# Performance work log

Hardware: AMD Instinct MI355X
Metric: run time of the kernel (lower is better)

Reference implementation:

```python
import jax, jax.numpy as jnp
import numpy as np

N, E, F_IN, HEADS, OUT_PER_HEAD = 50000, 1600000, 128, 4, 32
NEG_SLOPE = 0.2  # LeakyReLU slope used by standard GATConv


def setup_inputs() -> dict:
    key = jax.random.key(0)
    ks = jax.random.split(key, 7)
    x = jax.random.normal(ks[0], (N, F_IN), dtype=jnp.float32)
    edge_src = jax.random.randint(ks[1], (E,), 0, N, dtype=jnp.int64)
    edge_dst = jax.random.randint(ks[2], (E,), 0, N, dtype=jnp.int64)
    W = jax.random.normal(ks[3], (F_IN, HEADS * OUT_PER_HEAD), dtype=jnp.float32) / np.float32(np.sqrt(F_IN))
    a_src = jax.random.normal(ks[4], (HEADS, OUT_PER_HEAD), dtype=jnp.float32) * 0.1
    a_dst = jax.random.normal(ks[5], (HEADS, OUT_PER_HEAD), dtype=jnp.float32) * 0.1
    bias = jnp.zeros((HEADS * OUT_PER_HEAD,), dtype=jnp.float32)
    return {"x": x, "W": W, "a_src": a_src, "a_dst": a_dst, "bias": bias,
            "edge_src": edge_src, "edge_dst": edge_dst}


def reference(x, W, a_src, a_dst, bias, edge_src, edge_dst):
    # GATConv with concat=True over a static edge list (the faithful
    # static-shape form of tf.where(adj>0.5) -> gather -> GAT -> scatter).
    n = x.shape[0]
    H, D = a_src.shape
    h = (x @ W).reshape(n, H, D)                      # [N,H,D] projected features
    # per-node attention logits for source / destination roles
    e_s = jnp.einsum('nhd,hd->nh', h, a_src)          # [N,H]
    e_d = jnp.einsum('nhd,hd->nh', h, a_dst)          # [N,H]
    # per-edge logits with LeakyReLU
    e = jax.nn.leaky_relu(e_s[edge_src] + e_d[edge_dst], NEG_SLOPE)  # [E,H]
    # numerically stable softmax over incoming edges of each destination node
    m = jax.ops.segment_max(e, edge_dst, num_segments=n)             # [N,H]
    m = jnp.where(jnp.isfinite(m), m, 0.0)
    alpha = jnp.exp(e - m[edge_dst])                                 # [E,H]
    denom = jax.ops.segment_sum(alpha, edge_dst, num_segments=n)     # [N,H]
    alpha = alpha / jnp.where(denom > 0, denom, 1.0)[edge_dst]
    # weighted aggregation of source features onto destinations
    msgs = alpha[:, :, None] * h[edge_src]                           # [E,H,D]
    out = jax.ops.segment_sum(msgs, edge_dst, num_segments=n)        # [N,H,D]
    return out.reshape(n, H * D) + bias
```

## Files before the change

### kernel.cpp

```cpp
#include <hip/hip_runtime.h>
#include <math.h>

#define NEG_SLOPE 0.2f
#define NB1 256
#define XROW 136
#define BSHIFT 4
#define BNODES 16
#define CAP 1024
#define NBUCK_MAX 3200

typedef __attribute__((ext_vector_type(8))) short short8;
typedef __attribute__((ext_vector_type(4))) float floatx4;

__device__ __forceinline__ unsigned short f2bf(float f) {
    unsigned int u = __float_as_uint(f);
    u += 0x7fffu + ((u >> 16) & 1u);
    return (unsigned short)(u >> 16);
}
__device__ __forceinline__ float bf2f(unsigned short b) {
    return __uint_as_float(((unsigned int)b) << 16);
}
__device__ __forceinline__ float u2fl(unsigned int u) {
    return __uint_as_float(u << 16);
}
__device__ __forceinline__ float u2fh(unsigned int u) {
    return __uint_as_float(u & 0xffff0000u);
}

__device__ __forceinline__ void fma8(float* a, int o, float wt, const uint4& hv) {
    a[o + 0] = fmaf(wt, u2fl(hv.x), a[o + 0]);
    a[o + 1] = fmaf(wt, u2fh(hv.x), a[o + 1]);
    a[o + 2] = fmaf(wt, u2fl(hv.y), a[o + 2]);
    a[o + 3] = fmaf(wt, u2fh(hv.y), a[o + 3]);
    a[o + 4] = fmaf(wt, u2fl(hv.z), a[o + 4]);
    a[o + 5] = fmaf(wt, u2fh(hv.z), a[o + 5]);
    a[o + 6] = fmaf(wt, u2fl(hv.w), a[o + 6]);
    a[o + 7] = fmaf(wt, u2fh(hv.w), a[o + 7]);
}

__global__ __launch_bounds__(256) void prep_w_kernel(
    const float* __restrict__ W, unsigned short* __restrict__ WThi,
    unsigned short* __restrict__ WTlo, int* __restrict__ gcur, int nbuck)
{
    const int idx = blockIdx.x * 256 + threadIdx.x;
    const int j = idx >> 7, k = idx & 127;
    const float w = W[k * 128 + j];
    const unsigned short hi = f2bf(w);
    const unsigned short lo = f2bf(w - bf2f(hi));
    WThi[idx] = hi;
    WTlo[idx] = lo;
    if (idx < nbuck) gcur[idx] = idx * CAP;
}

__global__ __launch_bounds__(256) void fused_gemm_scatter(
    const float* __restrict__ x, const unsigned short* __restrict__ WThi,
    const unsigned short* __restrict__ WTlo, const float* __restrict__ a_src,
    const float* __restrict__ a_dst, unsigned short* __restrict__ hb,
    float* __restrict__ es, float* __restrict__ ed, int n,
    const int* __restrict__ src, const int* __restrict__ dst,
    int* __restrict__ gcur, int* __restrict__ ebuf, int e, int nbuck)
{
    __shared__ union {
        struct { unsigned short Xhi[32 * XROW]; unsigned short Xlo[32 * XROW]; } g;
        int cnt[NBUCK_MAX];
    } sm;

    const int t = threadIdx.x;

    if (blockIdx.x < NB1) {
        for (int b = t; b < nbuck; b += 256) sm.cnt[b] = 0;
        __syncthreads();
        const int per = (e + NB1 - 1) / NB1;
        const int lo = blockIdx.x * per;
        const int m = min(e, lo + per) - lo;
        for (int j = t; j < m; j += 256)
            atomicAdd(&sm.cnt[dst[lo + j] >> BSHIFT], 1);
        __syncthreads();
        for (int b = t; b < nbuck; b += 256) {
            const int c = sm.cnt[b];
            if (c > 0) sm.cnt[b] = atomicAdd(&gcur[b], c);
        }
        __syncthreads();
        for (int j = t; j < m; j += 256) {
            const int d = dst[lo + j];
            const int pos = atomicAdd(&sm.cnt[d >> BSHIFT], 1);
            ebuf[pos] = src[lo + j] | ((d & (BNODES - 1)) << 16);
        }
        return;
    }

    const int wv = t >> 6, lane = t & 63;
    const int l16 = lane & 15, quad = lane >> 4;
    const int node_base = (blockIdx.x - NB1) * 32;

    short8 bh[4][2], bl[4][2];
    #pragma unroll
    for (int c = 0; c < 4; ++c) {
        #pragma unroll
        for (int u = 0; u < 2; ++u) {
            const int j = (wv * 2 + u) * 16 + l16;
            const int ko = c * 32 + quad * 8;
            bh[c][u] = *(const short8*)&WThi[j * 128 + ko];
            bl[c][u] = *(const short8*)&WTlo[j * 128 + ko];
        }
    }

    for (int i = t; i < 1024; i += 256) {
        const int nd = i >> 5;
        const int k4 = i & 31;
        float4 xv = make_float4(0.f, 0.f, 0.f, 0.f);
        if (node_base + nd < n)
            xv = ((const float4*)(x + (size_t)(node_base + nd) * 128))[k4];
        const unsigned short h0 = f2bf(xv.x), h1 = f2bf(xv.y),
                             h2 = f2bf(xv.z), h3 = f2bf(xv.w);
        const unsigned short l0 = f2bf(xv.x - bf2f(h0)), l1 = f2bf(xv.y - bf2f(h1)),
                             l2 = f2bf(xv.z - bf2f(h2)), l3 = f2bf(xv.w - bf2f(h3));
        *(ushort4*)&sm.g.Xhi[nd * XROW + k4 * 4] = make_ushort4(h0, h1, h2, h3);
        *(ushort4*)&sm.g.Xlo[nd * XROW + k4 * 4] = make_ushort4(l0, l1, l2, l3);
    }
    __syncthreads();

    floatx4 acc[2][2] = {};
    #pragma unroll
    for (int c = 0; c < 4; ++c) {
        const int ko = c * 32 + quad * 8;
        short8 ah[2], al[2];
        #pragma unroll
        for (int r = 0; r < 2; ++r) {
            ah[r] = *(const short8*)&sm.g.Xhi[(r * 16 + l16) * XROW + ko];
            al[r] = *(const short8*)&sm.g.Xlo[(r * 16 + l16) * XROW + ko];
        }
        #pragma unroll
        for (int r = 0; r < 2; ++r)
        #pragma unroll
        for (int u = 0; u < 2; ++u) {
            acc[r][u] = __builtin_amdgcn_mfma_f32_16x16x32_bf16(ah[r], bl[c][u], acc[r][u], 0, 0, 0);
            acc[r][u] = __builtin_amdgcn_mfma_f32_16x16x32_bf16(al[r], bh[c][u], acc[r][u], 0, 0, 0);
            acc[r][u] = __builtin_amdgcn_mfma_f32_16x16x32_bf16(ah[r], bh[c][u], acc[r][u], 0, 0, 0);
        }
    }

    float asv[2], adv[2];
    #pragma unroll
    for (int u = 0; u < 2; ++u) {
        const int feat = (wv * 2 + u) * 16 + l16;
        asv[u] = a_src[feat];
        adv[u] = a_dst[feat];
    }
    #pragma unroll
    for (int r = 0; r < 2; ++r) {
        #pragma unroll
        for (int u = 0; u < 2; ++u) {
            const int feat = (wv * 2 + u) * 16 + l16;
            #pragma unroll
            for (int g = 0; g < 4; ++g) {
                const int node = node_base + r * 16 + quad * 4 + g;
                if (node < n)
                    hb[(size_t)node * 128 + feat] = f2bf(acc[r][u][g]);
            }
        }
        #pragma unroll
        for (int g = 0; g < 4; ++g) {
            float ps = acc[r][0][g] * asv[0] + acc[r][1][g] * asv[1];
            float pd = acc[r][0][g] * adv[0] + acc[r][1][g] * adv[1];
            #pragma unroll
            for (int o = 8; o >= 1; o >>= 1) {
                ps += __shfl_xor(ps, o);
                pd += __shfl_xor(pd, o);
            }
            const int node = node_base + r * 16 + quad * 4 + g;
            if (l16 == 0 && node < n) {
                es[node * 4 + wv] = ps;
                ed[node * 4 + wv] = pd;
            }
        }
    }
}

__global__ __launch_bounds__(256) void sort_agg_kernel(
    const unsigned short* __restrict__ hb, const float* __restrict__ es,
    const float* __restrict__ ed, const float* __restrict__ bias,
    const int* __restrict__ gcur, const int* __restrict__ ebuf,
    float* __restrict__ out, int n)
{
    __shared__ unsigned short esort[CAP];
    __shared__ int hist[BNODES], hexcl[BNODES], cur[BNODES];
    const int b = blockIdx.x;
    const int t = threadIdx.x;
    const int lane = t & 63;
    const int wv = t >> 6;
    const int l8 = lane & 7;
    const int oct = lane >> 3;
    const int f0 = l8 * 16;
    const int hh = l8 >> 1;

    const int start = b * CAP;
    const int end = gcur[b];

    if (t < BNODES) hist[t] = 0;
    __syncthreads();
    for (int i = start + t; i < end; i += 256)
        atomicAdd(&hist[(ebuf[i] >> 16) & (BNODES - 1)], 1);
    __syncthreads();
    if (wv == 0) {
        const int v = (lane < BNODES) ? hist[lane] : 0;
        int incl = v;
        #pragma unroll
        for (int o = 1; o < BNODES; o <<= 1) {
            const int tt = __shfl_up(incl, o);
            if (lane >= o) incl += tt;
        }
        if (lane < BNODES) { hexcl[lane] = incl - v; cur[lane] = incl - v; }
    }
    __syncthreads();
    for (int i = start + t; i < end; i += 256) {
        const int v = ebuf[i];
        const int pos = atomicAdd(&cur[(v >> 16) & (BNODES - 1)], 1);
        esort[pos] = (unsigned short)(v & 0xFFFF);
    }
    __syncthreads();

    for (int j = 0; j < 4; ++j) {
        const int nd = wv * 4 + j;
        const int node = b * BNODES + nd;
        if (node >= n) break;
        const int off = hexcl[nd];
        const int deg = hist[nd];
        const float edh = ed[(size_t)node * 4 + hh];

        float a[16];
        #pragma unroll
        for (int k = 0; k < 16; ++k) a[k] = 0.f;
        float wsum = 0.f;

        for (int c0 = 0; c0 < deg; c0 += 16) {
            const int ci0 = c0 + oct;
            const int ci1 = ci0 + 8;
            const int dm = deg - 1;
            const int s0 = esort[off + min(ci0, dm)];
            const int s1 = esort[off + min(ci1, dm)];
            const float e0 = es[(size_t)s0 * 4 + hh];
            const float e1 = es[(size_t)s1 * 4 + hh];
            const uint4 hA0 = *(const uint4*)&hb[(size_t)s0 * 128 + f0];
            const uint4 hB0 = *(const uint4*)&hb[(size_t)s0 * 128 + f0 + 8];
            const uint4 hA1 = *(const uint4*)&hb[(size_t)s1 * 128 + f0];
            const uint4 hB1 = *(const uint4*)&hb[(size_t)s1 * 128 + f0 + 8];
            float lg0 = e0 + edh; lg0 = lg0 > 0.f ? lg0 : NEG_SLOPE * lg0;
            float lg1 = e1 + edh; lg1 = lg1 > 0.f ? lg1 : NEG_SLOPE * lg1;
            const float w0 = (ci0 < deg) ? __expf(lg0) : 0.f;
            const float w1 = (ci1 < deg) ? __expf(lg1) : 0.f;
            fma8(a, 0, w0, hA0); fma8(a, 8, w0, hB0);
            fma8(a, 0, w1, hA1); fma8(a, 8, w1, hB1);
            wsum += w0 + w1;
        }
        #pragma unroll
        for (int o = 8; o <= 32; o <<= 1) {
            #pragma unroll
            for (int k = 0; k < 16; ++k) a[k] += __shfl_xor(a[k], o);
            wsum += __shfl_xor(wsum, o);
        }
        if (oct == 0) {
            const float inv = 1.f / ((wsum > 0.f) ? wsum : 1.f);
            #pragma unroll
            for (int q = 0; q < 4; ++q) {
                const float4 bq = *(const float4*)(bias + f0 + q * 4);
                float4 o4;
                o4.x = a[q * 4 + 0] * inv + bq.x;
                o4.y = a[q * 4 + 1] * inv + bq.y;
                o4.z = a[q * 4 + 2] * inv + bq.z;
                o4.w = a[q * 4 + 3] * inv + bq.w;
                *(float4*)(out + (size_t)node * 128 + f0 + q * 4) = o4;
            }
        }
    }
}

extern "C" void kernel_launch(void* const* d_in, const int* in_sizes, int n_in,
                              void* d_out, int out_size, void* d_ws, size_t ws_size,
                              hipStream_t stream)
{
    const float* x      = (const float*)d_in[0];
    const float* W      = (const float*)d_in[1];
    const float* a_src  = (const float*)d_in[2];
    const float* a_dst  = (const float*)d_in[3];
    const float* bias   = (const float*)d_in[4];
    const int*   e_src  = (const int*)d_in[5];
    const int*   e_dst  = (const int*)d_in[6];
    float* out = (float*)d_out;

    const int n = in_sizes[0] / 128;
    const int e = in_sizes[5];
    const int nbuck = (n + BNODES - 1) >> BSHIFT;

    char* ws = (char*)d_ws;
    size_t o = 0;
    auto alloc = [&](size_t bytes) { void* p = ws + o; o += (bytes + 255) & ~(size_t)255; return p; };
    unsigned short* hb   = (unsigned short*)alloc((size_t)n * 128 * sizeof(unsigned short));
    unsigned short* WThi = (unsigned short*)alloc(128 * 128 * sizeof(unsigned short));
    unsigned short* WTlo = (unsigned short*)alloc(128 * 128 * sizeof(unsigned short));
    float* es      = (float*)alloc((size_t)n * 4 * sizeof(float));
    float* ed      = (float*)alloc((size_t)n * 4 * sizeof(float));
    int* gcur      = (int*)alloc((size_t)nbuck * sizeof(int));
    int* ebuf      = (int*)alloc((size_t)nbuck * CAP * sizeof(int));
    (void)ws_size; (void)n_in; (void)out_size;

    const int ngemm = (n + 31) / 32;
    prep_w_kernel<<<64, 256, 0, stream>>>(W, WThi, WTlo, gcur, nbuck);
    fused_gemm_scatter<<<NB1 + ngemm, 256, 0, stream>>>(x, WThi, WTlo, a_src, a_dst,
                                                        hb, es, ed, n,
                                                        e_src, e_dst, gcur, ebuf, e, nbuck);
    sort_agg_kernel<<<nbuck, 256, 0, stream>>>(hb, es, ed, bias, gcur, ebuf, out, n);
}
```

Before: 195.7 us.

## Replace shared-memory bucket histogram scatter with per-edge global atomics spread over all blocks

Edge bucketing no longer runs in 256 dedicated blocks that build a shared-memory histogram, reserve ranges with one global atomic per bucket, then scatter. Every block now does its GEMM tile and then bucket-scatters 1024 edges, using one global atomicAdd per edge on the bucket cursor. This spreads the scatter over far more blocks, drops the large shared histogram so occupancy can rise, and removes the three-phase barrier structure. In exchange it issues 1.6M contended global atomics instead of block-aggregated ones, and it makes the order of edges within each bucket nondeterministic.

```diff
diff --git a/kernel.cpp b/kernel.cpp
--- a/kernel.cpp
+++ b/kernel.cpp
@@ -2,12 +2,11 @@
 #include <math.h>
 
 #define NEG_SLOPE 0.2f
-#define NB1 256
 #define XROW 136
 #define BSHIFT 4
 #define BNODES 16
 #define CAP 1024
-#define NBUCK_MAX 3200
+#define EPB 1024
 
 typedef __attribute__((ext_vector_type(8))) short short8;
 typedef __attribute__((ext_vector_type(4))) float floatx4;
@@ -58,120 +57,120 @@
     const float* __restrict__ a_dst, unsigned short* __restrict__ hb,
     float* __restrict__ es, float* __restrict__ ed, int n,
     const int* __restrict__ src, const int* __restrict__ dst,
-    int* __restrict__ gcur, int* __restrict__ ebuf, int e, int nbuck)
+    int* __restrict__ gcur, int* __restrict__ ebuf, int e)
 {
-    __shared__ union {
-        struct { unsigned short Xhi[32 * XROW]; unsigned short Xlo[32 * XROW]; } g;
-        int cnt[NBUCK_MAX];
-    } sm;
-
+    __shared__ unsigned short Xhi[32 * XROW];
+    __shared__ unsigned short Xlo[32 * XROW];
     const int t = threadIdx.x;
-
-    if (blockIdx.x < NB1) {
-        for (int b = t; b < nbuck; b += 256) sm.cnt[b] = 0;
-        __syncthreads();
-        const int per = (e + NB1 - 1) / NB1;
-        const int lo = blockIdx.x * per;
-        const int m = min(e, lo + per) - lo;
-        for (int j = t; j < m; j += 256)
-            atomicAdd(&sm.cnt[dst[lo + j] >> BSHIFT], 1);
-        __syncthreads();
-        for (int b = t; b < nbuck; b += 256) {
-            const int c = sm.cnt[b];
-            if (c > 0) sm.cnt[b] = atomicAdd(&gcur[b], c);
-        }
-        __syncthreads();
-        for (int j = t; j < m; j += 256) {
-            const int d = dst[lo + j];
-            const int pos = atomicAdd(&sm.cnt[d >> BSHIFT], 1);
-            ebuf[pos] = src[lo + j] | ((d & (BNODES - 1)) << 16);
-        }
-        return;
-    }
-
     const int wv = t >> 6, lane = t & 63;
     const int l16 = lane & 15, quad = lane >> 4;
-    const int node_base = (blockIdx.x - NB1) * 32;
-
-    short8 bh[4][2], bl[4][2];
-    #pragma unroll
-    for (int c = 0; c < 4; ++c) {
-        #pragma unroll
-        for (int u = 0; u < 2; ++u) {
-            const int j = (wv * 2 + u) * 16 + l16;
+    const int node_base = blockIdx.x * 32;
+
+    if (node_base < n) {
+        short8 bh[4][2], bl[4][2];
+        #pragma unroll
+        for (int c = 0; c < 4; ++c) {
+            #pragma unroll
+            for (int u = 0; u < 2; ++u) {
+                const int j = (wv * 2 + u) * 16 + l16;
+                const int ko = c * 32 + quad * 8;
+                bh[c][u] = *(const short8*)&WThi[j * 128 + ko];
+                bl[c][u] = *(const short8*)&WTlo[j * 128 + ko];
+            }
+        }
+
+        for (int i = t; i < 1024; i += 256) {
+            const int nd = i >> 5;
+            const int k4 = i & 31;
+            float4 xv = make_float4(0.f, 0.f, 0.f, 0.f);
+            if (node_base + nd < n)
+                xv = ((const float4*)(x + (size_t)(node_base + nd) * 128))[k4];
+            const unsigned short h0 = f2bf(xv.x), h1 = f2bf(xv.y),
+                                 h2 = f2bf(xv.z), h3 = f2bf(xv.w);
+            const unsigned short l0 = f2bf(xv.x - bf2f(h0)), l1 = f2bf(xv.y - bf2f(h1)),
+                                 l2 = f2bf(xv.z - bf2f(h2)), l3 = f2bf(xv.w - bf2f(h3));
+            *(ushort4*)&Xhi[nd * XROW + k4 * 4] = make_ushort4(h0, h1, h2, h3);
+            *(ushort4*)&Xlo[nd * XROW + k4 * 4] = make_ushort4(l0, l1, l2, l3);
+        }
+        __syncthreads();
+
+        floatx4 acc[2][2] = {};
+        #pragma unroll
+        for (int c = 0; c < 4; ++c) {
             const int ko = c * 32 + quad * 8;
-            bh[c][u] = *(const short8*)&WThi[j * 128 + ko];
-            bl[c][u] = *(const short8*)&WTlo[j * 128 + ko];
-        }
-    }
-
-    for (int i = t; i < 1024; i += 256) {
-        const int nd = i >> 5;
-        const int k4 = i & 31;
-        float4 xv = make_float4(0.f, 0.f, 0.f, 0.f);
-        if (node_base + nd < n)
-            xv = ((const float4*)(x + (size_t)(node_base + nd) * 128))[k4];
-        const unsigned short h0 = f2bf(xv.x), h1 = f2bf(xv.y),
-                             h2 = f2bf(xv.z), h3 = f2bf(xv.w);
-        const unsigned short l0 = f2bf(xv.x - bf2f(h0)), l1 = f2bf(xv.y - bf2f(h1)),
-                             l2 = f2bf(xv.z - bf2f(h2)), l3 = f2bf(xv.w - bf2f(h3));
-        *(ushort4*)&sm.g.Xhi[nd * XROW + k4 * 4] = make_ushort4(h0, h1, h2, h3);
-        *(ushort4*)&sm.g.Xlo[nd * XROW + k4 * 4] = make_ushort4(l0, l1, l2, l3);
-    }
-    __syncthreads();
-
-    floatx4 acc[2][2] = {};
-    #pragma unroll
-    for (int c = 0; c < 4; ++c) {
-        const int ko = c * 32 + quad * 8;
-        short8 ah[2], al[2];
-        #pragma unroll
-        for (int r = 0; r < 2; ++r) {
-            ah[r] = *(const short8*)&sm.g.Xhi[(r * 16 + l16) * XROW + ko];
-            al[r] = *(const short8*)&sm.g.Xlo[(r * 16 + l16) * XROW + ko];
-        }
-        #pragma unroll
-        for (int r = 0; r < 2; ++r)
-        #pragma unroll
-        for (int u = 0; u < 2; ++u) {
-            acc[r][u] = __builtin_amdgcn_mfma_f32_16x16x32_bf16(ah[r], bl[c][u], acc[r][u], 0, 0, 0);
-            acc[r][u] = __builtin_amdgcn_mfma_f32_16x16x32_bf16(al[r], bh[c][u], acc[r][u], 0, 0, 0);
-            acc[r][u] = __builtin_amdgcn_mfma_f32_16x16x32_bf16(ah[r], bh[c][u], acc[r][u], 0, 0, 0);
-        }
-    }
-
-    float asv[2], adv[2];
-    #pragma unroll
-    for (int u = 0; u < 2; ++u) {
-        const int feat = (wv * 2 + u) * 16 + l16;
-        asv[u] = a_src[feat];
-        adv[u] = a_dst[feat];
-    }
-    #pragma unroll
-    for (int r = 0; r < 2; ++r) {
+            short8 ah[2], al[2];
+            #pragma unroll
+            for (int r = 0; r < 2; ++r) {
+                ah[r] = *(const short8*)&Xhi[(r * 16 + l16) * XROW + ko];
+                al[r] = *(const short8*)&Xlo[(r * 16 + l16) * XROW + ko];
+            }
+            #pragma unroll
+            for (int r = 0; r < 2; ++r)
+            #pragma unroll
+            for (int u = 0; u < 2; ++u) {
+                acc[r][u] = __builtin_amdgcn_mfma_f32_16x16x32_bf16(ah[r], bl[c][u], acc[r][u], 0, 0, 0);
+                acc[r][u] = __builtin_amdgcn_mfma_f32_16x16x32_bf16(al[r], bh[c][u], acc[r][u], 0, 0, 0);
+                acc[r][u] = __builtin_amdgcn_mfma_f32_16x16x32_bf16(ah[r], bh[c][u], acc[r][u], 0, 0, 0);
+            }
+        }
+
+        float asv[2], adv[2];
         #pragma unroll
         for (int u = 0; u < 2; ++u) {
             const int feat = (wv * 2 + u) * 16 + l16;
+            asv[u] = a_src[feat];
+            adv[u] = a_dst[feat];
+        }
+        #pragma unroll
+        for (int r = 0; r < 2; ++r) {
+            #pragma unroll
+            for (int u = 0; u < 2; ++u) {
+                const int feat = (wv * 2 + u) * 16 + l16;
+                #pragma unroll
+                for (int g = 0; g < 4; ++g) {
+                    const int node = node_base + r * 16 + quad * 4 + g;
+                    if (node < n)
+                        hb[(size_t)node * 128 + feat] = f2bf(acc[r][u][g]);
+                }
+            }
             #pragma unroll
             for (int g = 0; g < 4; ++g) {
+                float ps = acc[r][0][g] * asv[0] + acc[r][1][g] * asv[1];
+                float pd = acc[r][0][g] * adv[0] + acc[r][1][g] * adv[1];
+                #pragma unroll
+                for (int o = 8; o >= 1; o >>= 1) {
+                    ps += __shfl_xor(ps, o);
+                    pd += __shfl_xor(pd, o);
+                }
                 const int node = node_base + r * 16 + quad * 4 + g;
-                if (node < n)
-                    hb[(size_t)node * 128 + feat] = f2bf(acc[r][u][g]);
-            }
-        }
-        #pragma unroll
-        for (int g = 0; g < 4; ++g) {
-            float ps = acc[r][0][g] * asv[0] + acc[r][1][g] * asv[1];
-            float pd = acc[r][0][g] * adv[0] + acc[r][1][g] * adv[1];
-            #pragma unroll
-            for (int o = 8; o >= 1; o >>= 1) {
-                ps += __shfl_xor(ps, o);
-                pd += __shfl_xor(pd, o);
-            }
-            const int node = node_base + r * 16 + quad * 4 + g;
-            if (l16 == 0 && node < n) {
-                es[node * 4 + wv] = ps;
-                ed[node * 4 + wv] = pd;
+                if (l16 == 0 && node < n) {
+                    es[node * 4 + wv] = ps;
+                    ed[node * 4 + wv] = pd;
+                }
+            }
+        }
+    }
+
+    const int base = blockIdx.x * EPB;
+    if (base < e) {
+        const int i0 = base + t * 4;
+        if (i0 + 4 <= e) {
+            const int4 s4 = *(const int4*)(src + i0);
+            const int4 d4 = *(const int4*)(dst + i0);
+            int pos;
+            pos = atomicAdd(&gcur[d4.x >> BSHIFT], 1);
+            ebuf[pos] = s4.x | ((d4.x & (BNODES - 1)) << 16);
+            pos = atomicAdd(&gcur[d4.y >> BSHIFT], 1);
+            ebuf[pos] = s4.y | ((d4.y & (BNODES - 1)) << 16);
+            pos = atomicAdd(&gcur[d4.z >> BSHIFT], 1);
+            ebuf[pos] = s4.z | ((d4.z & (BNODES - 1)) << 16);
+            pos = atomicAdd(&gcur[d4.w >> BSHIFT], 1);
+            ebuf[pos] = s4.w | ((d4.w & (BNODES - 1)) << 16);
+        } else {
+            for (int i = i0; i < e && i < i0 + 4; ++i) {
+                const int d = dst[i];
+                const int pos = atomicAdd(&gcur[d >> BSHIFT], 1);
+                ebuf[pos] = src[i] | ((d & (BNODES - 1)) << 16);
             }
         }
     }
@@ -305,9 +304,11 @@
     (void)ws_size; (void)n_in; (void)out_size;
 
     const int ngemm = (n + 31) / 32;
+    const int nscat = (e + EPB - 1) / EPB;
+    const int nblk  = ngemm > nscat ? ngemm : nscat;
     prep_w_kernel<<<64, 256, 0, stream>>>(W, WThi, WTlo, gcur, nbuck);
-    fused_gemm_scatter<<<NB1 + ngemm, 256, 0, stream>>>(x, WThi, WTlo, a_src, a_dst,
-                                                        hb, es, ed, n,
-                                                        e_src, e_dst, gcur, ebuf, e, nbuck);
+    fused_gemm_scatter<<<nblk, 256, 0, stream>>>(x, WThi, WTlo, a_src, a_dst,
+                                                 hb, es, ed, n,
+                                                 e_src, e_dst, gcur, ebuf, e);
     sort_agg_kernel<<<nbuck, 256, 0, stream>>>(hb, es, ed, bias, gcur, ebuf, out, n);
 }
```

After: 291.5 us. 49.0% more time.

## Bucket edges into 256-node superbuckets and fuse scatter into every GEMM block

Applied to the files above, without the earlier changes.

The edge bucketing moves from 3125 buckets of 16 nodes, handled by 256 dedicated blocks, to 196 superbuckets of 256 nodes. Every GEMM block now also scatters a 4096-edge chunk. Edges are staged in LDS with vectorised int4 loads, and global cursors are padded to avoid false sharing. This cuts global atomic traffic and balances the scatter across all blocks. In exchange, each sort_agg block must scan its whole superbucket, about 16x more ebuf reads that it filters by sub-bucket. Overflow is now handled by clamping, which silently drops edges past capacity.

```diff
diff --git a/kernel.cpp b/kernel.cpp
--- a/kernel.cpp
+++ b/kernel.cpp
@@ -2,12 +2,13 @@
 #include <math.h>
 
 #define NEG_SLOPE 0.2f
-#define NB1 256
 #define XROW 136
-#define BSHIFT 4
 #define BNODES 16
-#define CAP 1024
-#define NBUCK_MAX 3200
+#define SBSHIFT 8
+#define NSB_MAX 256
+#define SCAP 8960
+#define CPAD 32
+#define EPB2 4096
 
 typedef __attribute__((ext_vector_type(8))) short short8;
 typedef __attribute__((ext_vector_type(4))) float floatx4;
@@ -25,6 +26,10 @@
 }
 __device__ __forceinline__ float u2fh(unsigned int u) {
     return __uint_as_float(u & 0xffff0000u);
+}
+__device__ __forceinline__ unsigned int pk(int s, int d) {
+    return (unsigned int)s | ((unsigned int)(d & 255) << 16)
+                           | ((unsigned int)(d >> SBSHIFT) << 24);
 }
 
 __device__ __forceinline__ void fma8(float* a, int o, float wt, const uint4& hv) {
@@ -40,7 +45,7 @@
 
 __global__ __launch_bounds__(256) void prep_w_kernel(
     const float* __restrict__ W, unsigned short* __restrict__ WThi,
-    unsigned short* __restrict__ WTlo, int* __restrict__ gcur, int nbuck)
+    unsigned short* __restrict__ WTlo, int* __restrict__ gcur, int nsb)
 {
     const int idx = blockIdx.x * 256 + threadIdx.x;
     const int j = idx >> 7, k = idx & 127;
@@ -49,7 +54,7 @@
     const unsigned short lo = f2bf(w - bf2f(hi));
     WThi[idx] = hi;
     WTlo[idx] = lo;
-    if (idx < nbuck) gcur[idx] = idx * CAP;
+    if (idx < nsb) gcur[idx * CPAD] = idx * SCAP;
 }
 
 __global__ __launch_bounds__(256) void fused_gemm_scatter(
@@ -58,120 +63,146 @@
     const float* __restrict__ a_dst, unsigned short* __restrict__ hb,
     float* __restrict__ es, float* __restrict__ ed, int n,
     const int* __restrict__ src, const int* __restrict__ dst,
-    int* __restrict__ gcur, int* __restrict__ ebuf, int e, int nbuck)
+    int* __restrict__ gcur, int* __restrict__ ebuf, int e, int nsb)
 {
     __shared__ union {
         struct { unsigned short Xhi[32 * XROW]; unsigned short Xlo[32 * XROW]; } g;
-        int cnt[NBUCK_MAX];
+        struct { unsigned int stash[EPB2]; int cnt[NSB_MAX]; int cur[NSB_MAX]; } s;
     } sm;
-
     const int t = threadIdx.x;
-
-    if (blockIdx.x < NB1) {
-        for (int b = t; b < nbuck; b += 256) sm.cnt[b] = 0;
-        __syncthreads();
-        const int per = (e + NB1 - 1) / NB1;
-        const int lo = blockIdx.x * per;
-        const int m = min(e, lo + per) - lo;
-        for (int j = t; j < m; j += 256)
-            atomicAdd(&sm.cnt[dst[lo + j] >> BSHIFT], 1);
-        __syncthreads();
-        for (int b = t; b < nbuck; b += 256) {
-            const int c = sm.cnt[b];
-            if (c > 0) sm.cnt[b] = atomicAdd(&gcur[b], c);
-        }
-        __syncthreads();
-        for (int j = t; j < m; j += 256) {
-            const int d = dst[lo + j];
-            const int pos = atomicAdd(&sm.cnt[d >> BSHIFT], 1);
-            ebuf[pos] = src[lo + j] | ((d & (BNODES - 1)) << 16);
-        }
-        return;
-    }
-
     const int wv = t >> 6, lane = t & 63;
     const int l16 = lane & 15, quad = lane >> 4;
-    const int node_base = (blockIdx.x - NB1) * 32;
-
-    short8 bh[4][2], bl[4][2];
-    #pragma unroll
-    for (int c = 0; c < 4; ++c) {
-        #pragma unroll
-        for (int u = 0; u < 2; ++u) {
-            const int j = (wv * 2 + u) * 16 + l16;
+    const int node_base = blockIdx.x * 32;
+
+    if (node_base < n) {
+        short8 bh[4][2], bl[4][2];
+        #pragma unroll
+        for (int c = 0; c < 4; ++c) {
+            #pragma unroll
+            for (int u = 0; u < 2; ++u) {
+                const int j = (wv * 2 + u) * 16 + l16;
+                const int ko = c * 32 + quad * 8;
+                bh[c][u] = *(const short8*)&WThi[j * 128 + ko];
+                bl[c][u] = *(const short8*)&WTlo[j * 128 + ko];
+            }
+        }
+
+        for (int i = t; i < 1024; i += 256) {
+            const int nd = i >> 5;
+            const int k4 = i & 31;
+            float4 xv = make_float4(0.f, 0.f, 0.f, 0.f);
+            if (node_base + nd < n)
+                xv = ((const float4*)(x + (size_t)(node_base + nd) * 128))[k4];
+            const unsigned short h0 = f2bf(xv.x), h1 = f2bf(xv.y),
+                                 h2 = f2bf(xv.z), h3 = f2bf(xv.w);
+            const unsigned short l0 = f2bf(xv.x - bf2f(h0)), l1 = f2bf(xv.y - bf2f(h1)),
+                                 l2 = f2bf(xv.z - bf2f(h2)), l3 = f2bf(xv.w - bf2f(h3));
+            *(ushort4*)&sm.g.Xhi[nd * XROW + k4 * 4] = make_ushort4(h0, h1, h2, h3);
+            *(ushort4*)&sm.g.Xlo[nd * XROW + k4 * 4] = make_ushort4(l0, l1, l2, l3);
+        }
+        __syncthreads();
+
+        floatx4 acc[2][2] = {};
+        #pragma unroll
+        for (int c = 0; c < 4; ++c) {
             const int ko = c * 32 + quad * 8;
-            bh[c][u] = *(const short8*)&WThi[j * 128 + ko];
-            bl[c][u] = *(const short8*)&WTlo[j * 128 + ko];
-        }
-    }
-
-    for (int i = t; i < 1024; i += 256) {
-        const int nd = i >> 5;
-        const int k4 = i & 31;
-        float4 xv = make_float4(0.f, 0.f, 0.f, 0.f);
-        if (node_base + nd < n)
-            xv = ((const float4*)(x + (size_t)(node_base + nd) * 128))[k4];
-        const unsigned short h0 = f2bf(xv.x), h1 = f2bf(xv.y),
-                             h2 = f2bf(xv.z), h3 = f2bf(xv.w);
-        const unsigned short l0 = f2bf(xv.x - bf2f(h0)), l1 = f2bf(xv.y - bf2f(h1)),
-                             l2 = f2bf(xv.z - bf2f(h2)), l3 = f2bf(xv.w - bf2f(h3));
-        *(ushort4*)&sm.g.Xhi[nd * XROW + k4 * 4] = make_ushort4(h0, h1, h2, h3);
-        *(ushort4*)&sm.g.Xlo[nd * XROW + k4 * 4] = make_ushort4(l0, l1, l2, l3);
-    }
-    __syncthreads();
-
-    floatx4 acc[2][2] = {};
-    #pragma unroll
-    for (int c = 0; c < 4; ++c) {
-        const int ko = c * 32 + quad * 8;
-        short8 ah[2], al[2];
-        #pragma unroll
-        for (int r = 0; r < 2; ++r) {
-            ah[r] = *(const short8*)&sm.g.Xhi[(r * 16 + l16) * XROW + ko];
-            al[r] = *(const short8*)&sm.g.Xlo[(r * 16 + l16) * XROW + ko];
-        }
-        #pragma unroll
-        for (int r = 0; r < 2; ++r)
-        #pragma unroll
-        for (int u = 0; u < 2; ++u) {
-            acc[r][u] = __builtin_amdgcn_mfma_f32_16x16x32_bf16(ah[r], bl[c][u], acc[r][u], 0, 0, 0);
-            acc[r][u] = __builtin_amdgcn_mfma_f32_16x16x32_bf16(al[r], bh[c][u], acc[r][u], 0, 0, 0);
-            acc[r][u] = __builtin_amdgcn_mfma_f32_16x16x32_bf16(ah[r], bh[c][u], acc[r][u], 0, 0, 0);
-        }
-    }
-
-    float asv[2], adv[2];
-    #pragma unroll
-    for (int u = 0; u < 2; ++u) {
-        const int feat = (wv * 2 + u) * 16 + l16;
-        asv[u] = a_src[feat];
-        adv[u] = a_dst[feat];
-    }
-    #pragma unroll
-    for (int r = 0; r < 2; ++r) {
+            short8 ah[2], al[2];
+            #pragma unroll
+            for (int r = 0; r < 2; ++r) {
+                ah[r] = *(const short8*)&sm.g.Xhi[(r * 16 + l16) * XROW + ko];
+                al[r] = *(const short8*)&sm.g.Xlo[(r * 16 + l16) * XROW + ko];
+            }
+            #pragma unroll
+            for (int r = 0; r < 2; ++r)
+            #pragma unroll
+            for (int u = 0; u < 2; ++u) {
+                acc[r][u] = __builtin_amdgcn_mfma_f32_16x16x32_bf16(ah[r], bl[c][u], acc[r][u], 0, 0, 0);
+                acc[r][u] = __builtin_amdgcn_mfma_f32_16x16x32_bf16(al[r], bh[c][u], acc[r][u], 0, 0, 0);
+                acc[r][u] = __builtin_amdgcn_mfma_f32_16x16x32_bf16(ah[r], bh[c][u], acc[r][u], 0, 0, 0);
+            }
+        }
+
+        float asv[2], adv[2];
         #pragma unroll
         for (int u = 0; u < 2; ++u) {
             const int feat = (wv * 2 + u) * 16 + l16;
+            asv[u] = a_src[feat];
+            adv[u] = a_dst[feat];
+        }
+        #pragma unroll
+        for (int r = 0; r < 2; ++r) {
+            #pragma unroll
+            for (int u = 0; u < 2; ++u) {
+                const int feat = (wv * 2 + u) * 16 + l16;
+                #pragma unroll
+                for (int g = 0; g < 4; ++g) {
+                    const int node = node_base + r * 16 + quad * 4 + g;
+                    if (node < n)
+                        hb[(size_t)node * 128 + feat] = f2bf(acc[r][u][g]);
+                }
+            }
             #pragma unroll
             for (int g = 0; g < 4; ++g) {
+                float ps = acc[r][0][g] * asv[0] + acc[r][1][g] * asv[1];
+                float pd = acc[r][0][g] * adv[0] + acc[r][1][g] * adv[1];
+                #pragma unroll
+                for (int o = 8; o >= 1; o >>= 1) {
+                    ps += __shfl_xor(ps, o);
+                    pd += __shfl_xor(pd, o);
+                }
                 const int node = node_base + r * 16 + quad * 4 + g;
-                if (node < n)
-                    hb[(size_t)node * 128 + feat] = f2bf(acc[r][u][g]);
-            }
-        }
-        #pragma unroll
-        for (int g = 0; g < 4; ++g) {
-            float ps = acc[r][0][g] * asv[0] + acc[r][1][g] * asv[1];
-            float pd = acc[r][0][g] * adv[0] + acc[r][1][g] * adv[1];
-            #pragma unroll
-            for (int o = 8; o >= 1; o >>= 1) {
-                ps += __shfl_xor(ps, o);
-                pd += __shfl_xor(pd, o);
-            }
-            const int node = node_base + r * 16 + quad * 4 + g;
-            if (l16 == 0 && node < n) {
-                es[node * 4 + wv] = ps;
-                ed[node * 4 + wv] = pd;
+                if (l16 == 0 && node < n) {
+                    es[node * 4 + wv] = ps;
+                    ed[node * 4 + wv] = pd;
+                }
+            }
+        }
+    }
+
+    const int base = blockIdx.x * EPB2;
+    if (base < e) {
+        __syncthreads();
+        for (int b = t; b < nsb; b += 256) sm.s.cnt[b] = 0;
+        __syncthreads();
+        const int m = min(e - base, EPB2);
+        #pragma unroll
+        for (int c = 0; c < 4; ++c) {
+            const int j0 = c * 1024 + t * 4;
+            if (j0 + 4 <= m) {
+                const int i0 = base + j0;
+                const int4 s4 = *(const int4*)(src + i0);
+                const int4 d4 = *(const int4*)(dst + i0);
+                sm.s.stash[j0 + 0] = pk(s4.x, d4.x);
+                atomicAdd(&sm.s.cnt[(unsigned)d4.x >> SBSHIFT], 1);
+                sm.s.stash[j0 + 1] = pk(s4.y, d4.y);
+                atomicAdd(&sm.s.cnt[(unsigned)d4.y >> SBSHIFT], 1);
+                sm.s.stash[j0 + 2] = pk(s4.z, d4.z);
+                atomicAdd(&sm.s.cnt[(unsigned)d4.z >> SBSHIFT], 1);
+                sm.s.stash[j0 + 3] = pk(s4.w, d4.w);
+                atomicAdd(&sm.s.cnt[(unsigned)d4.w >> SBSHIFT], 1);
+            } else if (j0 < m) {
+                for (int j = j0; j < m; ++j) {
+                    const int sv = src[base + j], dv = dst[base + j];
+                    sm.s.stash[j] = pk(sv, dv);
+                    atomicAdd(&sm.s.cnt[(unsigned)dv >> SBSHIFT], 1);
+                }
+            }
+        }
+        __syncthreads();
+        for (int b = t; b < nsb; b += 256) {
+            const int cc = sm.s.cnt[b];
+            sm.s.cur[b] = (cc > 0) ? atomicAdd(&gcur[b * CPAD], cc) : 0;
+        }
+        __syncthreads();
+        #pragma unroll
+        for (int c = 0; c < 4; ++c) {
+            const int j0 = c * 1024 + t * 4;
+            const int jend = min(j0 + 4, m);
+            for (int j = j0; j < jend; ++j) {
+                const unsigned int v = sm.s.stash[j];
+                const int sb = v >> 24;
+                const int pos = atomicAdd(&sm.s.cur[sb], 1);
+                if (pos < (sb + 1) * SCAP) ebuf[pos] = (int)v;
             }
         }
     }
@@ -183,7 +214,7 @@
     const int* __restrict__ gcur, const int* __restrict__ ebuf,
     float* __restrict__ out, int n)
 {
-    __shared__ unsigned short esort[CAP];
+    __shared__ unsigned short esort[1024];
     __shared__ int hist[BNODES], hexcl[BNODES], cur[BNODES];
     const int b = blockIdx.x;
     const int t = threadIdx.x;
@@ -193,14 +224,18 @@
     const int oct = lane >> 3;
     const int f0 = l8 * 16;
     const int hh = l8 >> 1;
-
-    const int start = b * CAP;
-    const int end = gcur[b];
+    const int s = b >> 4;
+    const unsigned int sub = b & 15;
+    const int rb = s * SCAP;
+    const int rcount = min(gcur[s * CPAD] - rb, SCAP);
 
     if (t < BNODES) hist[t] = 0;
     __syncthreads();
-    for (int i = start + t; i < end; i += 256)
-        atomicAdd(&hist[(ebuf[i] >> 16) & (BNODES - 1)], 1);
+    for (int i = t; i < rcount; i += 256) {
+        const unsigned int v = (unsigned int)ebuf[rb + i];
+        if (((v >> 20) & 15u) == sub)
+            atomicAdd(&hist[(v >> 16) & 15u], 1);
+    }
     __syncthreads();
     if (wv == 0) {
         const int v = (lane < BNODES) ? hist[lane] : 0;
@@ -213,10 +248,12 @@
         if (lane < BNODES) { hexcl[lane] = incl - v; cur[lane] = incl - v; }
     }
     __syncthreads();
-    for (int i = start + t; i < end; i += 256) {
-        const int v = ebuf[i];
-        const int pos = atomicAdd(&cur[(v >> 16) & (BNODES - 1)], 1);
-        esort[pos] = (unsigned short)(v & 0xFFFF);
+    for (int i = t; i < rcount; i += 256) {
+        const unsigned int v = (unsigned int)ebuf[rb + i];
+        if (((v >> 20) & 15u) == sub) {
+            const int pos = atomicAdd(&cur[(v >> 16) & 15u], 1);
+            if (pos < 1024) esort[pos] = (unsigned short)(v & 0xFFFFu);
+        }
     }
     __syncthreads();
 
@@ -237,8 +274,8 @@
             const int ci0 = c0 + oct;
             const int ci1 = ci0 + 8;
             const int dm = deg - 1;
-            const int s0 = esort[off + min(ci0, dm)];
-            const int s1 = esort[off + min(ci1, dm)];
+            const int s0 = esort[min(off + min(ci0, dm), 1023)];
+            const int s1 = esort[min(off + min(ci1, dm), 1023)];
             const float e0 = es[(size_t)s0 * 4 + hh];
             const float e1 = es[(size_t)s1 * 4 + hh];
             const uint4 hA0 = *(const uint4*)&hb[(size_t)s0 * 128 + f0];
@@ -290,7 +327,8 @@
 
     const int n = in_sizes[0] / 128;
     const int e = in_sizes[5];
-    const int nbuck = (n + BNODES - 1) >> BSHIFT;
+    const int nbuck = (n + BNODES - 1) / BNODES;
+    const int nsb = (n + 255) >> SBSHIFT;
 
     char* ws = (char*)d_ws;
     size_t o = 0;
@@ -300,14 +338,16 @@
     unsigned short* WTlo = (unsigned short*)alloc(128 * 128 * sizeof(unsigned short));
     float* es      = (float*)alloc((size_t)n * 4 * sizeof(float));
     float* ed      = (float*)alloc((size_t)n * 4 * sizeof(float));
-    int* gcur      = (int*)alloc((size_t)nbuck * sizeof(int));
-    int* ebuf      = (int*)alloc((size_t)nbuck * CAP * sizeof(int));
+    int* gcur      = (int*)alloc((size_t)nsb * CPAD * sizeof(int));
+    int* ebuf      = (int*)alloc((size_t)nsb * SCAP * sizeof(int));
     (void)ws_size; (void)n_in; (void)out_size;
 
     const int ngemm = (n + 31) / 32;
-    prep_w_kernel<<<64, 256, 0, stream>>>(W, WThi, WTlo, gcur, nbuck);
-    fused_gemm_scatter<<<NB1 + ngemm, 256, 0, stream>>>(x, WThi, WTlo, a_src, a_dst,
-                                                        hb, es, ed, n,
-                                                        e_src, e_dst, gcur, ebuf, e, nbuck);
+    const int nscat = (e + EPB2 - 1) / EPB2;
+    const int nblk  = ngemm > nscat ? ngemm : nscat;
+    prep_w_kernel<<<64, 256, 0, stream>>>(W, WThi, WTlo, gcur, nsb);
+    fused_gemm_scatter<<<nblk, 256, 0, stream>>>(x, WThi, WTlo, a_src, a_dst,
+                                                 hb, es, ed, n,
+                                                 e_src, e_dst, gcur, ebuf, e, nsb);
     sort_agg_kernel<<<nbuck, 256, 0, stream>>>(hb, es, ed, bias, gcur, ebuf, out, n);
 }
```

After: 227.2 us. +16.1%, slower.
